# Performance work log

Measured on AMD Instinct MI355X. Metric: run time of the kernel, lower is better.

Reference implementation:

```python
import jax, jax.numpy as jnp
import numpy as np

EPS = 1e-6
D, L, HEADS, FF = 384, 12, 6, 1536


def _ln(x, w, b):
    m = x.mean(-1, keepdims=True)
    v = ((x - m) ** 2).mean(-1, keepdims=True)
    return (x - m) / jnp.sqrt(v + EPS) * w + b


def setup_inputs() -> dict:
    key = jax.random.key(0)
    ks = iter(jax.random.split(key, 16))
    B, Cin, H, W = 16, 7, 192, 640
    N = (H // 16) * (W // 16) + 1  # 481 tokens

    def w(shape, s=0.02):
        return (jax.random.normal(next(ks), shape, jnp.float32) * s)

    return dict(
        input=jax.random.normal(next(ks), (B, Cin, H, W), jnp.float32),
        conv_w=w((D, Cin, 16, 16)),
        conv_b=jnp.zeros((D,), jnp.float32),
        cls_token=w((1, 1, D)),
        pos_embed=w((1, N, D)),
        ln1_w=jnp.ones((L, D), jnp.float32), ln1_b=jnp.zeros((L, D), jnp.float32),
        qkv_w=w((L, 3 * D, D)), qkv_b=jnp.zeros((L, 3 * D), jnp.float32),
        proj_w=w((L, D, D)), proj_b=jnp.zeros((L, D), jnp.float32),
        ln2_w=jnp.ones((L, D), jnp.float32), ln2_b=jnp.zeros((L, D), jnp.float32),
        fc1_w=w((L, FF, D)), fc1_b=jnp.zeros((L, FF), jnp.float32),
        fc2_w=w((L, D, FF)), fc2_b=jnp.zeros((L, D), jnp.float32),
        norm_w=jnp.ones((D,), jnp.float32), norm_b=jnp.zeros((D,), jnp.float32),
        to_qkv_w=w((3 * D, D)),
        pose_w=w((D, D)), pose_b=jnp.zeros((D,), jnp.float32),
    )


def reference(input, conv_w, conv_b, cls_token, pos_embed, ln1_w, ln1_b,
              qkv_w, qkv_b, proj_w, proj_b, ln2_w, ln2_b, fc1_w, fc1_b,
              fc2_w, fc2_b, norm_w, norm_b, to_qkv_w, pose_w, pose_b):
    B = input.shape[0]
    dh = D // HEADS
    # patch embed: conv stride=kernel=16 -> [B,384,12,40] -> [B,480,384]
    x = jax.lax.conv_general_dilated(
        input, conv_w, (16, 16), 'VALID',
        dimension_numbers=('NCHW', 'OIHW', 'NCHW')) + conv_b[None, :, None, None]
    x = x.reshape(B, D, -1).transpose(0, 2, 1)
    x = jnp.concatenate([jnp.broadcast_to(cls_token, (B, 1, D)), x], axis=1) + pos_embed
    # 12 pre-norm ViT blocks (timm vit_small: 6 heads, GELU, eps=1e-6)
    for i in range(L):
        h = _ln(x, ln1_w[i], ln1_b[i])
        qkv = h @ qkv_w[i].T + qkv_b[i]
        q, k, v = jnp.split(qkv, 3, axis=-1)
        hd = lambda t: t.reshape(B, -1, HEADS, dh).transpose(0, 2, 1, 3)
        q, k, v = hd(q) * (dh ** -0.5), hd(k), hd(v)
        a = jax.nn.softmax(jnp.einsum('bhqd,bhkd->bhqk', q, k), axis=-1)
        o = jnp.einsum('bhqk,bhkd->bhqd', a, v).transpose(0, 2, 1, 3).reshape(B, -1, D)
        x = x + o @ proj_w[i].T + proj_b[i]
        h = _ln(x, ln2_w[i], ln2_b[i])
        h = jax.nn.gelu(h @ fc1_w[i].T + fc1_b[i], approximate=False)
        x = x + h @ fc2_w[i].T + fc2_b[i]
    x = _ln(x, norm_w, norm_b)
    # ---- make_pose (training branch: per-column-chunk softmax + median mask) ----
    t = x[:, 1:, :]                      # drop cls -> [B,480,384]
    N = t.shape[1]
    qkv = (t @ to_qkv_w.T).reshape(B, N, 3, D).transpose(2, 0, 1, 3)
    q, k, v = qkv[0] * 0.05103, qkv[1], qkv[2]
    attn = jnp.einsum('bqc,bkc->bqk', q, k) / 100.0
    # col chunk c = columns {c + 40*j : j=0..11}; 40 disjoint chunks of 12
    col_idx = jnp.arange(40)[:, None] + 40 * jnp.arange(12)[None, :]  # [40,12]
    part = jax.nn.softmax(attn[:, :, col_idx], axis=-1)               # [B,N,40,12]
    # torch.median of 12 values = lower median = sorted index (12-1)//2
    med = jnp.sort(part, axis=-1)[..., (12 - 1) // 2][..., None]
    mask = jnp.where(part > med, 0.0, part)
    flat_cols = col_idx.reshape(-1)  # permutation of 0..479
    attn_new = jnp.zeros_like(attn).at[:, :, flat_cols].set(part.reshape(B, N, N))
    masked = jnp.zeros_like(attn).at[:, :, flat_cols].set(mask.reshape(B, N, N))
    masked = masked / ((D // 8) / 2)  # /= num_indices/2 = 24
    # NOTE: einsum 'bal,bnc->bac' shares only 'b': rowsum(attn) outer rowsum(v)
    out = jnp.einsum('bal,bnc->bac', attn_new, v)
    out = out @ pose_w.T + pose_b
    out = _ln(out, norm_w, norm_b)
    attn_map = attn_new.mean(axis=1).reshape(B, 12, 40)
    masked_map = masked.mean(axis=1).reshape(B, 12, 40)
    return out.mean(axis=1), attn_map, masked_map
```

## Files before the change

kernel.cpp:

```cpp
#include <hip/hip_runtime.h>
#include <hip/hip_bf16.h>

#define TD 384
#define NHEAD 6
#define NFF 1536
#define NB 16
#define NTOK 481
#define NROWS (NB*NTOK)

typedef __attribute__((ext_vector_type(8))) __bf16 bf16x8;
typedef __attribute__((ext_vector_type(4))) __bf16 bf16x4;
typedef __attribute__((ext_vector_type(4))) float f32x4;

static __device__ __forceinline__ float gelu_f(float v){
    return 0.5f*v*(1.0f + erff(v*0.70710678118654752f));
}

static __device__ __forceinline__ void gload16(const void* g, void* l){
    __builtin_amdgcn_global_load_lds((const __attribute__((address_space(1))) void*)g,
                                     (__attribute__((address_space(3))) void*)l, 16, 0, 0);
}

template<int ROWS>
static __device__ __forceinline__ void stageT(const __bf16* g, int ldel, __bf16* lds, int w, int lane){
    #pragma unroll
    for (int j = 0; j < ROWS/32; ++j){
        int i = w*(ROWS/32) + j;
        int ol = i*1024 + lane*16;
        int row = ol >> 7, colb = ol & 127;
        int sc = colb ^ ((row & 7) << 4);
        gload16((const char*)g + (long)row*ldel*2 + sc, (char*)lds + i*1024);
    }
}

__global__ __launch_bounds__(256) void mgemm(
    const __bf16* __restrict__ A, int lda, long sA,
    const __bf16* __restrict__ Bm, int ldb, long sB,
    void* __restrict__ Cp, int ldc, long sC,
    const float* __restrict__ bias,
    const float* __restrict__ Rp, long sR,
    int M, int N, int K, float scale, int act, int obf)
{
    __shared__ __align__(16) __bf16 As[2][64*64];
    __shared__ __align__(16) __bf16 Bs[2][64*64];
    const int bz = blockIdx.z;
    A  += (long)bz*sA; Bm += (long)bz*sB;

    const int nwg = gridDim.x*gridDim.y;
    const int id  = blockIdx.y*gridDim.x + blockIdx.x;
    const int q8  = nwg >> 3, r8 = nwg & 7;
    const int xcd = id & 7, sub = id >> 3;
    const int nid = (xcd < r8 ? xcd*(q8+1) : r8*(q8+1) + (xcd-r8)*q8) + sub;
    const int m0 = (nid / gridDim.x) * 64, n0 = (nid % gridDim.x) * 64;

    const int tid = threadIdx.x;
    const int w = tid >> 6, lane = tid & 63;
    const int wr = w >> 1, wc = w & 1;
    const int lr = lane & 15, lg = lane >> 4;

    f32x4 acc[2][2];
    #pragma unroll
    for (int m=0;m<2;++m)
        #pragma unroll
        for (int n=0;n<2;++n)
            acc[m][n] = (f32x4){0.f,0.f,0.f,0.f};

    const __bf16* Ag = A + (long)m0*lda;
    const __bf16* Bg = Bm + (long)n0*ldb;
    const int NT = K >> 6;

    stageT<64>(Ag, lda, As[0], w, lane);
    stageT<64>(Bg, ldb, Bs[0], w, lane);
    int cur = 0;
    for (int t = 0; t < NT; ++t){
        if (t+1 < NT){
            stageT<64>(Ag + (t+1)*64, lda, As[cur^1], w, lane);
            stageT<64>(Bg + (t+1)*64, ldb, Bs[cur^1], w, lane);
            asm volatile("s_waitcnt vmcnt(4)" ::: "memory");
        } else {
            asm volatile("s_waitcnt vmcnt(0)" ::: "memory");
        }
        __builtin_amdgcn_sched_barrier(0);
        __builtin_amdgcn_s_barrier();
        #pragma unroll
        for (int kk=0;kk<2;++kk){
            const int sa = ((kk*64 + lg*16) ^ ((lr&7)<<4));
            bf16x8 af[2], bfr[2];
            #pragma unroll
            for (int m=0;m<2;++m)
                af[m] = *(const bf16x8*)((const char*)&As[cur][0] + (wr*32 + m*16 + lr)*128 + sa);
            #pragma unroll
            for (int n=0;n<2;++n)
                bfr[n] = *(const bf16x8*)((const char*)&Bs[cur][0] + (wc*32 + n*16 + lr)*128 + sa);
            #pragma unroll
            for (int m=0;m<2;++m)
                #pragma unroll
                for (int n=0;n<2;++n)
                    acc[m][n] = __builtin_amdgcn_mfma_f32_16x16x32_bf16(af[m], bfr[n], acc[m][n], 0, 0, 0);
        }
        __builtin_amdgcn_s_barrier();
        cur ^= 1;
    }

    #pragma unroll
    for (int m=0;m<2;++m){
        #pragma unroll
        for (int n=0;n<2;++n){
            int col = n0 + wc*32 + n*16 + lr;
            if (col >= N) continue;
            #pragma unroll
            for (int e=0;e<4;++e){
                int row = m0 + wr*32 + m*16 + lg*4 + e;
                if (row >= M) continue;
                float v = acc[m][n][e]*scale;
                if (bias) v += bias[col];
                if (act) v = gelu_f(v);
                if (Rp) v += Rp[(long)bz*sR + (long)row*ldc + col];
                if (obf) ((__bf16*)Cp)[(long)bz*sC + (long)row*ldc + col] = (__bf16)v;
                else     ((float*)Cp)[(long)bz*sC + (long)row*ldc + col] = v;
            }
        }
    }
}

__global__ __launch_bounds__(256) void attn2(const __bf16* __restrict__ QKV, __bf16* __restrict__ O)
{
    __shared__ __align__(16) __bf16 Ks[64*64];
    __shared__ __align__(16) __bf16 VT[64*72];
    __shared__ __align__(16) __bf16 Ps[64*72];
    const int qt=blockIdx.x, h=blockIdx.y, b=blockIdx.z;
    const int tid=threadIdx.x, w=tid>>6, lane=tid&63;
    const int lr=lane&15, lg=lane>>4;
    const __bf16* base = QKV + (long)b*NTOK*1152;
    const long qrow = qt*64 + w*16 + lr;
    const bf16x8 qa0 = *(const bf16x8*)(base + qrow*1152 + h*64 + lg*8);
    const bf16x8 qa1 = *(const bf16x8*)(base + qrow*1152 + h*64 + 32 + lg*8);

    f32x4 oacc[4];
    float mo[4], lo[4];
    #pragma unroll
    for (int e=0;e<4;++e){ mo[e]=-1e30f; lo[e]=0.f; }
    #pragma unroll
    for (int n=0;n<4;++n) oacc[n]=(f32x4){0.f,0.f,0.f,0.f};

    for (int kt=0; kt<8; ++kt){
        __syncthreads();
        #pragma unroll
        for (int j=0;j<2;++j){
            int i = w*2+j;
            int ol = i*1024 + lane*16;
            int row = ol>>7, colb = ol&127;
            int sc = colb ^ ((row&7)<<4);
            gload16((const char*)base + ((long)(kt*64+row)*1152 + 384 + h*64)*2 + sc,
                    (char*)Ks + i*1024);
        }
        #pragma unroll
        for (int rep=0;rep<2;++rep){
            int c = tid + rep*256;
            int kv = c & 63, d8 = c >> 6;
            bf16x8 vv = *(const bf16x8*)(base + (long)(kt*64+kv)*1152 + 768 + h*64 + d8*8);
            #pragma unroll
            for (int jj=0;jj<8;++jj) VT[(d8*8+jj)*72 + kv] = vv[jj];
        }
        __syncthreads();

        f32x4 s[4];
        #pragma unroll
        for (int n=0;n<4;++n) s[n]=(f32x4){0.f,0.f,0.f,0.f};
        #pragma unroll
        for (int kk=0;kk<2;++kk){
            const int sa = ((kk*64 + lg*16) ^ ((lr&7)<<4));
            #pragma unroll
            for (int n=0;n<4;++n){
                bf16x8 kb = *(const bf16x8*)((const char*)Ks + (n*16+lr)*128 + sa);
                s[n] = __builtin_amdgcn_mfma_f32_16x16x32_bf16(kk? qa1:qa0, kb, s[n], 0,0,0);
            }
        }
        #pragma unroll
        for (int n=0;n<4;++n){
            int col = kt*64 + n*16 + lr;
            bool bad = col >= NTOK;
            #pragma unroll
            for (int e=0;e<4;++e) s[n][e] = bad ? -1e30f : s[n][e]*0.125f;
        }
        #pragma unroll
        for (int e=0;e<4;++e){
            float rm = fmaxf(fmaxf(s[0][e],s[1][e]), fmaxf(s[2][e],s[3][e]));
            rm = fmaxf(rm, __shfl_xor(rm,1));
            rm = fmaxf(rm, __shfl_xor(rm,2));
            rm = fmaxf(rm, __shfl_xor(rm,4));
            rm = fmaxf(rm, __shfl_xor(rm,8));
            float mn = fmaxf(mo[e], rm);
            float al = __expf(mo[e]-mn);
            float rs = 0.f;
            #pragma unroll
            for (int n=0;n<4;++n){ float p=__expf(s[n][e]-mn); s[n][e]=p; rs+=p; }
            rs += __shfl_xor(rs,1); rs += __shfl_xor(rs,2);
            rs += __shfl_xor(rs,4); rs += __shfl_xor(rs,8);
            lo[e] = lo[e]*al + rs; mo[e]=mn;
            #pragma unroll
            for (int n=0;n<4;++n) oacc[n][e] *= al;
        }
        #pragma unroll
        for (int n=0;n<4;++n)
            #pragma unroll
            for (int e=0;e<4;++e)
                Ps[(w*16+lg*4+e)*72 + n*16+lr] = (__bf16)s[n][e];
        #pragma unroll
        for (int kk=0;kk<2;++kk){
            bf16x8 pa = *(const bf16x8*)&Ps[(w*16+lr)*72 + kk*32 + lg*8];
            #pragma unroll
            for (int n=0;n<4;++n){
                bf16x8 vf = *(const bf16x8*)&VT[(n*16+lr)*72 + kk*32 + lg*8];
                oacc[n] = __builtin_amdgcn_mfma_f32_16x16x32_bf16(pa, vf, oacc[n], 0,0,0);
            }
        }
    }
    #pragma unroll
    for (int e=0;e<4;++e){
        int q = qt*64 + w*16 + lg*4 + e;
        if (q < NTOK){
            float inv = 1.f/lo[e];
            __bf16* op = O + ((long)b*NTOK + q)*TD + h*64;
            #pragma unroll
            for (int n=0;n<4;++n)
                op[n*16+lr] = (__bf16)(oacc[n][e]*inv);
        }
    }
}

__global__ __launch_bounds__(128) void ln_kernel(const float* __restrict__ Xp, __bf16* __restrict__ Y,
    const float* __restrict__ W, const float* __restrict__ Bp)
{
    long r = blockIdx.x;
    int t = threadIdx.x;
    const float* x = Xp + r*TD;
    float v0 = x[t], v1 = x[t+128], v2 = x[t+256];
    float s = v0+v1+v2;
    float q = v0*v0+v1*v1+v2*v2;
    #pragma unroll
    for (int w=1; w<64; w<<=1){ s += __shfl_xor(s,w); q += __shfl_xor(q,w); }
    __shared__ float sm[2][2];
    if ((t&63)==0){ sm[t>>6][0]=s; sm[t>>6][1]=q; }
    __syncthreads();
    float S = sm[0][0]+sm[1][0];
    float Q = sm[0][1]+sm[1][1];
    float mean = S*(1.f/384.f);
    float var  = Q*(1.f/384.f) - mean*mean;
    float rstd = rsqrtf(var + 1e-6f);
    __bf16* y = Y + r*TD;
    y[t]     = (__bf16)((v0-mean)*rstd*W[t]     + Bp[t]);
    y[t+128] = (__bf16)((v1-mean)*rstd*W[t+128] + Bp[t+128]);
    y[t+256] = (__bf16)((v2-mean)*rstd*W[t+256] + Bp[t+256]);
}

__global__ void wconv_kernel(const float* __restrict__ s, __bf16* __restrict__ d, int n4){
    int i = blockIdx.x*256 + threadIdx.x;
    if (i < n4){
        float4 v = ((const float4*)s)[i];
        bf16x4 p; p[0]=(__bf16)v.x; p[1]=(__bf16)v.y; p[2]=(__bf16)v.z; p[3]=(__bf16)v.w;
        ((bf16x4*)d)[i] = p;
    }
}

__global__ void im2col_kernel(const float* __restrict__ in, __bf16* __restrict__ outp)
{
    long idx = (long)blockIdx.x*256 + threadIdx.x;
    if (idx >= (long)7680*1792) return;
    int k = (int)(idx % 1792);
    long m = idx / 1792;
    int pw = (int)(m % 40);
    long t2 = m / 40;
    int ph = (int)(t2 % 12);
    int b  = (int)(t2 / 12);
    int kw = k & 15, kh = (k >> 4) & 15, c = k >> 8;
    outp[idx] = (__bf16)in[(((long)(b*7 + c)*192) + ph*16 + kh)*640 + pw*16 + kw];
}

__global__ void assemble_kernel(const float* __restrict__ CO, const float* __restrict__ cls,
    const float* __restrict__ pos, float* __restrict__ X)
{
    long idx = (long)blockIdx.x*256 + threadIdx.x;
    if (idx >= (long)NROWS*TD) return;
    int d = (int)(idx % TD);
    long r = idx / TD;
    int tok = (int)(r % NTOK);
    int b   = (int)(r / NTOK);
    float v = (tok == 0) ? cls[d] : CO[((long)b*480 + tok-1)*TD + d];
    X[idx] = v + pos[tok*TD + d];
}

__global__ __launch_bounds__(256) void pose_maps_kernel(const float* __restrict__ PA,
    float* __restrict__ attn_map, float* __restrict__ masked_map)
{
    int i = blockIdx.x;
    int b = blockIdx.y;
    int t = threadIdx.x;
    float accA[12], accM[12];
    #pragma unroll
    for (int j=0;j<12;++j){ accA[j]=0.f; accM[j]=0.f; }
    for (int a = t; a < 480; a += 256) {
        const float* row = PA + ((long)(b*480 + a))*480 + i;
        float v[12];
        float mx = -1e30f;
        #pragma unroll
        for (int j=0;j<12;++j){ v[j] = row[40*j]; mx = fmaxf(mx, v[j]); }
        float sum = 0.f;
        #pragma unroll
        for (int j=0;j<12;++j){ v[j] = expf(v[j]-mx); sum += v[j]; }
        float invs = 1.f/sum;
        #pragma unroll
        for (int j=0;j<12;++j) v[j] *= invs;
        float srt[12];
        #pragma unroll
        for (int j=0;j<12;++j){
            float x = v[j]; int p = j;
            while (p > 0 && srt[p-1] > x){ srt[p]=srt[p-1]; --p; }
            srt[p]=x;
        }
        float med = srt[5];
        #pragma unroll
        for (int j=0;j<12;++j){
            accA[j] += v[j];
            accM[j] += (v[j] > med) ? 0.f : v[j];
        }
    }
    __shared__ float redA[256*12];
    __shared__ float redM[256*12];
    #pragma unroll
    for (int j=0;j<12;++j){ redA[t*12+j]=accA[j]; redM[t*12+j]=accM[j]; }
    __syncthreads();
    for (int sgap=128; sgap>0; sgap>>=1){
        if (t < sgap){
            #pragma unroll
            for (int j=0;j<12;++j){
                redA[t*12+j] += redA[(t+sgap)*12+j];
                redM[t*12+j] += redM[(t+sgap)*12+j];
            }
        }
        __syncthreads();
    }
    if (t < 12){
        attn_map  [(b*12 + t)*40 + i] = redA[t] * (1.f/480.f);
        masked_map[(b*12 + t)*40 + i] = redM[t] * (1.f/480.f) * (1.f/24.f);
    }
}

__global__ __launch_bounds__(384) void colsum4_kernel(const __bf16* __restrict__ QKV2, float* __restrict__ CS4)
{
    int b = blockIdx.x, j = blockIdx.y, c = threadIdx.x;
    const __bf16* p = QKV2 + (long)b*480*1152 + 768 + c;
    float s = 0.f;
    for (int a = j*120; a < j*120+120; ++a) s += (float)p[(long)a*1152];
    CS4[((long)b*4 + j)*384 + c] = s;
}

__global__ __launch_bounds__(384) void pose_final_kernel(const float* __restrict__ CS4,
    const float* __restrict__ PW, const float* __restrict__ PB,
    const float* __restrict__ NW, const float* __restrict__ NBb, float* __restrict__ out)
{
    int b = blockIdx.x, c = threadIdx.x;
    const float* s0 = CS4 + (long)b*1536;
    __shared__ float sv[384];
    sv[c] = s0[c] + s0[384+c] + s0[768+c] + s0[1152+c];
    __syncthreads();
    const float* wr = PW + (long)c*384;
    float acc = 0.f;
    for (int k = 0; k < 384; ++k) acc += sv[k]*wr[k];
    acc = 40.f*acc + PB[c];
    float s = acc, q = acc*acc;
    #pragma unroll
    for (int w=1; w<64; w<<=1){ s += __shfl_xor(s,w); q += __shfl_xor(q,w); }
    __shared__ float sm[6][2];
    if ((c & 63) == 0){ sm[c>>6][0]=s; sm[c>>6][1]=q; }
    __syncthreads();
    float S=0.f, Q=0.f;
    for (int i=0;i<6;++i){ S+=sm[i][0]; Q+=sm[i][1]; }
    float mean = S*(1.f/384.f);
    float var  = Q*(1.f/384.f) - mean*mean;
    float rstd = rsqrtf(var + 1e-6f);
    out[b*384 + c] = (acc-mean)*rstd*NW[c] + NBb[c];
}

extern "C" void kernel_launch(void* const* d_in, const int* in_sizes, int n_in,
                              void* d_out, int out_size, void* d_ws, size_t ws_size,
                              hipStream_t stream)
{
    const float* input  = (const float*)d_in[0];
    const float* conv_w = (const float*)d_in[1];
    const float* conv_b = (const float*)d_in[2];
    const float* cls    = (const float*)d_in[3];
    const float* pos    = (const float*)d_in[4];
    const float* ln1w   = (const float*)d_in[5];
    const float* ln1b   = (const float*)d_in[6];
    const float* qkvw   = (const float*)d_in[7];
    const float* qkvb   = (const float*)d_in[8];
    const float* projw  = (const float*)d_in[9];
    const float* projb  = (const float*)d_in[10];
    const float* ln2w   = (const float*)d_in[11];
    const float* ln2b   = (const float*)d_in[12];
    const float* fc1w   = (const float*)d_in[13];
    const float* fc1b   = (const float*)d_in[14];
    const float* fc2w   = (const float*)d_in[15];
    const float* fc2b   = (const float*)d_in[16];
    const float* normw  = (const float*)d_in[17];
    const float* normb  = (const float*)d_in[18];
    const float* toqkvw = (const float*)d_in[19];
    const float* posew  = (const float*)d_in[20];
    const float* poseb  = (const float*)d_in[21];
    float* out = (float*)d_out;
    float* ws  = (float*)d_ws;

    __bf16* WB   = (__bf16*)ws;
    float*  X    = ws + 11182080;
    __bf16* Hbf  = (__bf16*)(ws + 14137344);
    __bf16* QKVb = (__bf16*)(ws + 15636480);
    __bf16* Obuf = (__bf16*)(ws + 21633024);
    float*  PAb  = ws + 23132160;
    float*  CS4  = PAb + 3686400;
    __bf16* IM2C = QKVb;

    __bf16* Wconv = WB;
    __bf16* Wqkv  = WB + 688128;
    __bf16* Wproj = WB + 5996544;
    __bf16* Wfc1  = WB + 7766016;
    __bf16* Wfc2  = WB + 14843904;
    __bf16* Wtoq  = WB + 21921792;

    wconv_kernel<<<dim3((172032+255)/256), 256, 0, stream>>>(conv_w, Wconv, 172032);
    wconv_kernel<<<dim3((1327104+255)/256), 256, 0, stream>>>(qkvw,  Wqkv, 1327104);
    wconv_kernel<<<dim3((442368+255)/256), 256, 0, stream>>>(projw, Wproj, 442368);
    wconv_kernel<<<dim3((1769472+255)/256), 256, 0, stream>>>(fc1w,  Wfc1, 1769472);
    wconv_kernel<<<dim3((1769472+255)/256), 256, 0, stream>>>(fc2w,  Wfc2, 1769472);
    wconv_kernel<<<dim3((110592+255)/256), 256, 0, stream>>>(toqkvw, Wtoq, 110592);

    {
        long total = (long)7680*1792;
        im2col_kernel<<<dim3((unsigned)((total+255)/256)), 256, 0, stream>>>(input, IM2C);
    }
    mgemm<<<dim3(6, 120, 1), 256, 0, stream>>>(IM2C, 1792, 0, Wconv, 1792, 0,
        PAb, 384, 0, conv_b, nullptr, 0, 7680, 384, 1792, 1.f, 0, 0);
    assemble_kernel<<<dim3((NROWS*TD+255)/256), 256, 0, stream>>>(PAb, cls, pos, X);

    for (int i = 0; i < 12; ++i) {
        ln_kernel<<<dim3(NROWS), 128, 0, stream>>>(X, Hbf, ln1w + i*384, ln1b + i*384);
        mgemm<<<dim3(18, 121, 1), 256, 0, stream>>>(Hbf, 384, 0, Wqkv + (long)i*1152*384, 384, 0,
            QKVb, 1152, 0, qkvb + i*1152, nullptr, 0, NROWS, 1152, 384, 1.f, 0, 1);
        attn2<<<dim3(8, NHEAD, NB), 256, 0, stream>>>(QKVb, Obuf);
        mgemm<<<dim3(6, 121, 1), 256, 0, stream>>>(Obuf, 384, 0, Wproj + (long)i*384*384, 384, 0,
            X, 384, 0, projb + i*384, X, 0, NROWS, 384, 384, 1.f, 0, 0);
        ln_kernel<<<dim3(NROWS), 128, 0, stream>>>(X, Hbf, ln2w + i*384, ln2b + i*384);
        mgemm<<<dim3(24, 121, 1), 256, 0, stream>>>(Hbf, 384, 0, Wfc1 + (long)i*1536*384, 384, 0,
            QKVb, 1536, 0, fc1b + i*1536, nullptr, 0, NROWS, 1536, 384, 1.f, 1, 1);
        mgemm<<<dim3(6, 121, 1), 256, 0, stream>>>(QKVb, 1536, 0, Wfc2 + (long)i*384*1536, 1536, 0,
            X, 384, 0, fc2b + i*384, X, 0, NROWS, 384, 1536, 1.f, 0, 0);
    }
    ln_kernel<<<dim3(NROWS), 128, 0, stream>>>(X, Hbf, normw, normb);

    mgemm<<<dim3(18, 8, 16), 256, 0, stream>>>(Hbf + 384, 384, (long)481*384,
        Wtoq, 384, 0, QKVb, 1152, (long)480*1152, nullptr, nullptr, 0, 480, 1152, 384, 1.f, 0, 1);
    mgemm<<<dim3(8, 8, 16), 256, 0, stream>>>(QKVb, 1152, (long)480*1152,
        QKVb + 384, 1152, (long)480*1152, PAb, 480, (long)480*480, nullptr, nullptr, 0,
        480, 480, 384, 0.05103f*0.01f, 0, 0);
    pose_maps_kernel<<<dim3(40, 16), 256, 0, stream>>>(PAb, out + 6144, out + 13824);
    colsum4_kernel<<<dim3(16, 4), 384, 0, stream>>>(QKVb, CS4);
    pose_final_kernel<<<dim3(16), 384, 0, stream>>>(CS4, posew, poseb, normw, normb, out);
}
```

Before: 1.805 ms.

## Fold LayerNorm into GEMM epilogues and double-buffer K/V loads in attention

LayerNorm weights are folded into the QKV, FC1 and to_qkv weight matrices. The mean and rstd correction is applied in the GEMM epilogue from per-row stats computed by a light stats kernel over a bf16 copy of the residual stream, which the residual GEMMs now also write. This drops the separate normalized-activation write and read each layer. The attention kernel also double-buffers K tiles and prefetches V into registers to overlap loads with MFMA compute. The risk is precision: the GEMM now consumes unnormalized bf16 activations, and the mean subtraction happens after accumulation, so cancellation can occur.

```diff
diff --git a/kernel.cpp b/kernel.cpp
--- a/kernel.cpp
+++ b/kernel.cpp
@@ -39,6 +39,8 @@
     void* __restrict__ Cp, int ldc, long sC,
     const float* __restrict__ bias,
     const float* __restrict__ Rp, long sR,
+    const float2* __restrict__ MR, long sMR, const float2* __restrict__ SB2,
+    __bf16* __restrict__ Xbp,
     int M, int N, int K, float scale, int act, int obf)
 {
     __shared__ __align__(16) __bf16 As[2][64*64];
@@ -105,19 +107,27 @@
     #pragma unroll
     for (int m=0;m<2;++m){
         #pragma unroll
-        for (int n=0;n<2;++n){
-            int col = n0 + wc*32 + n*16 + lr;
-            if (col >= N) continue;
-            #pragma unroll
-            for (int e=0;e<4;++e){
-                int row = m0 + wr*32 + m*16 + lg*4 + e;
-                if (row >= M) continue;
-                float v = acc[m][n][e]*scale;
-                if (bias) v += bias[col];
+        for (int e=0;e<4;++e){
+            int row = m0 + wr*32 + m*16 + lg*4 + e;
+            if (row >= M) continue;
+            float2 mr = MR ? MR[(long)bz*sMR + row] : make_float2(0.f,0.f);
+            #pragma unroll
+            for (int n=0;n<2;++n){
+                int col = n0 + wc*32 + n*16 + lr;
+                if (col >= N) continue;
+                float v = acc[m][n][e];
+                if (MR){
+                    float2 sb = SB2[col];
+                    v = mr.y*(v - mr.x*sb.x) + sb.y;
+                } else {
+                    v = v*scale;
+                    if (bias) v += bias[col];
+                }
                 if (act) v = gelu_f(v);
                 if (Rp) v += Rp[(long)bz*sR + (long)row*ldc + col];
                 if (obf) ((__bf16*)Cp)[(long)bz*sC + (long)row*ldc + col] = (__bf16)v;
                 else     ((float*)Cp)[(long)bz*sC + (long)row*ldc + col] = v;
+                if (Xbp) Xbp[(long)row*ldc + col] = (__bf16)v;
             }
         }
     }
@@ -125,17 +135,29 @@
 
 __global__ __launch_bounds__(256) void attn2(const __bf16* __restrict__ QKV, __bf16* __restrict__ O)
 {
-    __shared__ __align__(16) __bf16 Ks[64*64];
+    __shared__ __align__(16) __bf16 Ks[2][64*64];
     __shared__ __align__(16) __bf16 VT[64*72];
     __shared__ __align__(16) __bf16 Ps[64*72];
     const int qt=blockIdx.x, h=blockIdx.y, b=blockIdx.z;
     const int tid=threadIdx.x, w=tid>>6, lane=tid&63;
     const int lr=lane&15, lg=lane>>4;
+    const int kv0 = tid & 63, d80 = tid >> 6;
     const __bf16* base = QKV + (long)b*NTOK*1152;
     const long qrow = qt*64 + w*16 + lr;
     const bf16x8 qa0 = *(const bf16x8*)(base + qrow*1152 + h*64 + lg*8);
     const bf16x8 qa1 = *(const bf16x8*)(base + qrow*1152 + h*64 + 32 + lg*8);
 
+    #pragma unroll
+    for (int j=0;j<2;++j){
+        int i = w*2+j;
+        int ol = i*1024 + lane*16;
+        int row = ol>>7, colb = ol&127;
+        int sc = colb ^ ((row&7)<<4);
+        gload16((const char*)base + ((long)row*1152 + 384 + h*64)*2 + sc, (char*)Ks[0] + i*1024);
+    }
+    bf16x8 vv0 = *(const bf16x8*)(base + (long)kv0*1152 + 768 + h*64 + d80*8);
+    bf16x8 vv1 = *(const bf16x8*)(base + (long)kv0*1152 + 768 + h*64 + (d80+4)*8);
+
     f32x4 oacc[4];
     float mo[4], lo[4];
     #pragma unroll
@@ -143,26 +165,30 @@
     #pragma unroll
     for (int n=0;n<4;++n) oacc[n]=(f32x4){0.f,0.f,0.f,0.f};
 
+    int cur = 0;
     for (int kt=0; kt<8; ++kt){
-        __syncthreads();
-        #pragma unroll
-        for (int j=0;j<2;++j){
-            int i = w*2+j;
-            int ol = i*1024 + lane*16;
-            int row = ol>>7, colb = ol&127;
-            int sc = colb ^ ((row&7)<<4);
-            gload16((const char*)base + ((long)(kt*64+row)*1152 + 384 + h*64)*2 + sc,
-                    (char*)Ks + i*1024);
-        }
-        #pragma unroll
-        for (int rep=0;rep<2;++rep){
-            int c = tid + rep*256;
-            int kv = c & 63, d8 = c >> 6;
-            bf16x8 vv = *(const bf16x8*)(base + (long)(kt*64+kv)*1152 + 768 + h*64 + d8*8);
-            #pragma unroll
-            for (int jj=0;jj<8;++jj) VT[(d8*8+jj)*72 + kv] = vv[jj];
-        }
-        __syncthreads();
+        asm volatile("s_waitcnt vmcnt(0)" ::: "memory");
+        __builtin_amdgcn_sched_barrier(0);
+        #pragma unroll
+        for (int jj=0;jj<8;++jj) VT[(d80*8+jj)*72 + kv0] = vv0[jj];
+        #pragma unroll
+        for (int jj=0;jj<8;++jj) VT[((d80+4)*8+jj)*72 + kv0] = vv1[jj];
+        if (kt+1 < 8){
+            #pragma unroll
+            for (int j=0;j<2;++j){
+                int i = w*2+j;
+                int ol = i*1024 + lane*16;
+                int row = ol>>7, colb = ol&127;
+                int sc = colb ^ ((row&7)<<4);
+                gload16((const char*)base + ((long)((kt+1)*64+row)*1152 + 384 + h*64)*2 + sc,
+                        (char*)Ks[cur^1] + i*1024);
+            }
+            vv0 = *(const bf16x8*)(base + (long)((kt+1)*64+kv0)*1152 + 768 + h*64 + d80*8);
+            vv1 = *(const bf16x8*)(base + (long)((kt+1)*64+kv0)*1152 + 768 + h*64 + (d80+4)*8);
+        }
+        asm volatile("s_waitcnt lgkmcnt(0)" ::: "memory");
+        __builtin_amdgcn_sched_barrier(0);
+        __builtin_amdgcn_s_barrier();
 
         f32x4 s[4];
         #pragma unroll
@@ -172,7 +198,7 @@
             const int sa = ((kk*64 + lg*16) ^ ((lr&7)<<4));
             #pragma unroll
             for (int n=0;n<4;++n){
-                bf16x8 kb = *(const bf16x8*)((const char*)Ks + (n*16+lr)*128 + sa);
+                bf16x8 kb = *(const bf16x8*)((const char*)&Ks[cur][0] + (n*16+lr)*128 + sa);
                 s[n] = __builtin_amdgcn_mfma_f32_16x16x32_bf16(kk? qa1:qa0, kb, s[n], 0,0,0);
             }
         }
@@ -215,6 +241,8 @@
                 oacc[n] = __builtin_amdgcn_mfma_f32_16x16x32_bf16(pa, vf, oacc[n], 0,0,0);
             }
         }
+        __builtin_amdgcn_s_barrier();
+        cur ^= 1;
     }
     #pragma unroll
     for (int e=0;e<4;++e){
@@ -229,29 +257,63 @@
     }
 }
 
-__global__ __launch_bounds__(128) void ln_kernel(const float* __restrict__ Xp, __bf16* __restrict__ Y,
-    const float* __restrict__ W, const float* __restrict__ Bp)
-{
-    long r = blockIdx.x;
-    int t = threadIdx.x;
-    const float* x = Xp + r*TD;
-    float v0 = x[t], v1 = x[t+128], v2 = x[t+256];
-    float s = v0+v1+v2;
-    float q = v0*v0+v1*v1+v2*v2;
-    #pragma unroll
-    for (int w=1; w<64; w<<=1){ s += __shfl_xor(s,w); q += __shfl_xor(q,w); }
-    __shared__ float sm[2][2];
-    if ((t&63)==0){ sm[t>>6][0]=s; sm[t>>6][1]=q; }
-    __syncthreads();
-    float S = sm[0][0]+sm[1][0];
-    float Q = sm[0][1]+sm[1][1];
-    float mean = S*(1.f/384.f);
-    float var  = Q*(1.f/384.f) - mean*mean;
-    float rstd = rsqrtf(var + 1e-6f);
-    __bf16* y = Y + r*TD;
-    y[t]     = (__bf16)((v0-mean)*rstd*W[t]     + Bp[t]);
-    y[t+128] = (__bf16)((v1-mean)*rstd*W[t+128] + Bp[t+128]);
-    y[t+256] = (__bf16)((v2-mean)*rstd*W[t+256] + Bp[t+256]);
+__global__ __launch_bounds__(256) void stats_kernel(const __bf16* __restrict__ Xb, float2* __restrict__ MR, int nrows)
+{
+    int row = blockIdx.x*4 + (threadIdx.x>>6);
+    if (row >= nrows) return;
+    int lane = threadIdx.x & 63;
+    const uint* p = (const uint*)(Xb + (long)row*384) + lane*3;
+    float s=0.f, q=0.f;
+    #pragma unroll
+    for (int i=0;i<3;++i){
+        uint u = p[i];
+        float a = __uint_as_float(u<<16);
+        float b = __uint_as_float(u & 0xFFFF0000u);
+        s += a+b; q += a*a + b*b;
+    }
+    #pragma unroll
+    for (int d=1; d<64; d<<=1){ s += __shfl_xor(s,d); q += __shfl_xor(q,d); }
+    if (lane==0){
+        float mu = s*(1.f/384.f);
+        float var = q*(1.f/384.f) - mu*mu;
+        MR[row] = make_float2(mu, rsqrtf(var + 1e-6f));
+    }
+}
+
+__global__ void wfold_kernel(const float* __restrict__ s, const float* __restrict__ lnw,
+                             __bf16* __restrict__ d, int n4, int per_layer4)
+{
+    int i = blockIdx.x*256 + threadIdx.x;
+    if (i >= n4) return;
+    int layer = i / per_layer4;
+    int k = (i*4) % 384;
+    float4 v = ((const float4*)s)[i];
+    const float4 lw = *(const float4*)(lnw + layer*384 + k);
+    bf16x4 p; p[0]=(__bf16)(v.x*lw.x); p[1]=(__bf16)(v.y*lw.y); p[2]=(__bf16)(v.z*lw.z); p[3]=(__bf16)(v.w*lw.w);
+    ((bf16x4*)d)[i] = p;
+}
+
+__global__ __launch_bounds__(256) void rowsum_kernel(const float* __restrict__ W,
+    const float* __restrict__ lnw, const float* __restrict__ lnb, const float* __restrict__ bias,
+    float2* __restrict__ SB2, int nrows, int rows_per_layer)
+{
+    int row = blockIdx.x*4 + (threadIdx.x>>6);
+    if (row >= nrows) return;
+    int lane = threadIdx.x & 63;
+    int layer = row / rows_per_layer;
+    const float* wr = W + (long)row*384;
+    const float* lw = lnw + layer*384;
+    const float* lb = lnb + layer*384;
+    float s=0.f, t=0.f;
+    #pragma unroll
+    for (int i=0;i<6;++i){
+        int k = lane + i*64;
+        float wv = wr[k];
+        s += lw[k]*wv; t += lb[k]*wv;
+    }
+    #pragma unroll
+    for (int d=1; d<64; d<<=1){ s += __shfl_xor(s,d); t += __shfl_xor(t,d); }
+    if (lane==0) SB2[row] = make_float2(s, bias ? t + bias[row] : t);
 }
 
 __global__ void wconv_kernel(const float* __restrict__ s, __bf16* __restrict__ d, int n4){
@@ -278,7 +340,7 @@
 }
 
 __global__ void assemble_kernel(const float* __restrict__ CO, const float* __restrict__ cls,
-    const float* __restrict__ pos, float* __restrict__ X)
+    const float* __restrict__ pos, float* __restrict__ X, __bf16* __restrict__ Xb)
 {
     long idx = (long)blockIdx.x*256 + threadIdx.x;
     if (idx >= (long)NROWS*TD) return;
@@ -287,7 +349,9 @@
     int tok = (int)(r % NTOK);
     int b   = (int)(r / NTOK);
     float v = (tok == 0) ? cls[d] : CO[((long)b*480 + tok-1)*TD + d];
-    X[idx] = v + pos[tok*TD + d];
+    v += pos[tok*TD + d];
+    X[idx] = v;
+    Xb[idx] = (__bf16)v;
 }
 
 __global__ __launch_bounds__(256) void pose_maps_kernel(const float* __restrict__ PA,
@@ -411,14 +475,18 @@
     float* out = (float*)d_out;
     float* ws  = (float*)d_ws;
 
-    __bf16* WB   = (__bf16*)ws;
-    float*  X    = ws + 11182080;
-    __bf16* Hbf  = (__bf16*)(ws + 14137344);
-    __bf16* QKVb = (__bf16*)(ws + 15636480);
-    __bf16* Obuf = (__bf16*)(ws + 21633024);
-    float*  PAb  = ws + 23132160;
-    float*  CS4  = PAb + 3686400;
-    __bf16* IM2C = QKVb;
+    __bf16* WB    = (__bf16*)ws;
+    float*  X     = ws + 11182080;
+    __bf16* Xb    = (__bf16*)(ws + 14137344);
+    __bf16* QKVb  = (__bf16*)(ws + 15636480);
+    __bf16* Obuf  = (__bf16*)(ws + 21633024);
+    float*  PAb   = ws + 23132160;
+    float*  CS4   = PAb + 3686400;
+    float2* MR    = (float2*)(ws + 26843136);
+    float2* SB2q  = (float2*)(ws + 26858752);
+    float2* SB2f  = (float2*)(ws + 26886400);
+    float2* SB2t  = (float2*)(ws + 26923264);
+    __bf16* IM2C  = QKVb;
 
     __bf16* Wconv = WB;
     __bf16* Wqkv  = WB + 688128;
@@ -428,40 +496,48 @@
     __bf16* Wtoq  = WB + 21921792;
 
     wconv_kernel<<<dim3((172032+255)/256), 256, 0, stream>>>(conv_w, Wconv, 172032);
-    wconv_kernel<<<dim3((1327104+255)/256), 256, 0, stream>>>(qkvw,  Wqkv, 1327104);
     wconv_kernel<<<dim3((442368+255)/256), 256, 0, stream>>>(projw, Wproj, 442368);
-    wconv_kernel<<<dim3((1769472+255)/256), 256, 0, stream>>>(fc1w,  Wfc1, 1769472);
     wconv_kernel<<<dim3((1769472+255)/256), 256, 0, stream>>>(fc2w,  Wfc2, 1769472);
-    wconv_kernel<<<dim3((110592+255)/256), 256, 0, stream>>>(toqkvw, Wtoq, 110592);
+    wfold_kernel<<<dim3((1327104+255)/256), 256, 0, stream>>>(qkvw, ln1w, Wqkv, 1327104, 110592);
+    wfold_kernel<<<dim3((1769472+255)/256), 256, 0, stream>>>(fc1w, ln2w, Wfc1, 1769472, 147456);
+    wfold_kernel<<<dim3((110592+255)/256), 256, 0, stream>>>(toqkvw, normw, Wtoq, 110592, 110592);
+    rowsum_kernel<<<dim3(13824/4), 256, 0, stream>>>(qkvw, ln1w, ln1b, qkvb, SB2q, 13824, 1152);
+    rowsum_kernel<<<dim3(18432/4), 256, 0, stream>>>(fc1w, ln2w, ln2b, fc1b, SB2f, 18432, 1536);
+    rowsum_kernel<<<dim3(1152/4), 256, 0, stream>>>(toqkvw, normw, normb, nullptr, SB2t, 1152, 1152);
 
     {
         long total = (long)7680*1792;
         im2col_kernel<<<dim3((unsigned)((total+255)/256)), 256, 0, stream>>>(input, IM2C);
     }
     mgemm<<<dim3(6, 120, 1), 256, 0, stream>>>(IM2C, 1792, 0, Wconv, 1792, 0,
-        PAb, 384, 0, conv_b, nullptr, 0, 7680, 384, 1792, 1.f, 0, 0);
-    assemble_kernel<<<dim3((NROWS*TD+255)/256), 256, 0, stream>>>(PAb, cls, pos, X);
+        PAb, 384, 0, conv_b, nullptr, 0, nullptr, 0, nullptr, nullptr, 7680, 384, 1792, 1.f, 0, 0);
+    assemble_kernel<<<dim3((NROWS*TD+255)/256), 256, 0, stream>>>(PAb, cls, pos, X, Xb);
 
     for (int i = 0; i < 12; ++i) {
-        ln_kernel<<<dim3(NROWS), 128, 0, stream>>>(X, Hbf, ln1w + i*384, ln1b + i*384);
-        mgemm<<<dim3(18, 121, 1), 256, 0, stream>>>(Hbf, 384, 0, Wqkv + (long)i*1152*384, 384, 0,
-            QKVb, 1152, 0, qkvb + i*1152, nullptr, 0, NROWS, 1152, 384, 1.f, 0, 1);
+        stats_kernel<<<dim3((NROWS+3)/4), 256, 0, stream>>>(Xb, MR, NROWS);
+        mgemm<<<dim3(18, 121, 1), 256, 0, stream>>>(Xb, 384, 0, Wqkv + (long)i*1152*384, 384, 0,
+            QKVb, 1152, 0, nullptr, nullptr, 0, MR, 0, SB2q + (long)i*1152, nullptr,
+            NROWS, 1152, 384, 1.f, 0, 1);
         attn2<<<dim3(8, NHEAD, NB), 256, 0, stream>>>(QKVb, Obuf);
         mgemm<<<dim3(6, 121, 1), 256, 0, stream>>>(Obuf, 384, 0, Wproj + (long)i*384*384, 384, 0,
-            X, 384, 0, projb + i*384, X, 0, NROWS, 384, 384, 1.f, 0, 0);
-        ln_kernel<<<dim3(NROWS), 128, 0, stream>>>(X, Hbf, ln2w + i*384, ln2b + i*384);
-        mgemm<<<dim3(24, 121, 1), 256, 0, stream>>>(Hbf, 384, 0, Wfc1 + (long)i*1536*384, 384, 0,
-            QKVb, 1536, 0, fc1b + i*1536, nullptr, 0, NROWS, 1536, 384, 1.f, 1, 1);
+            X, 384, 0, projb + i*384, X, 0, nullptr, 0, nullptr, Xb,
+            NROWS, 384, 384, 1.f, 0, 0);
+        stats_kernel<<<dim3((NROWS+3)/4), 256, 0, stream>>>(Xb, MR, NROWS);
+        mgemm<<<dim3(24, 121, 1), 256, 0, stream>>>(Xb, 384, 0, Wfc1 + (long)i*1536*384, 384, 0,
+            QKVb, 1536, 0, nullptr, nullptr, 0, MR, 0, SB2f + (long)i*1536, nullptr,
+            NROWS, 1536, 384, 1.f, 1, 1);
         mgemm<<<dim3(6, 121, 1), 256, 0, stream>>>(QKVb, 1536, 0, Wfc2 + (long)i*384*1536, 1536, 0,
-            X, 384, 0, fc2b + i*384, X, 0, NROWS, 384, 1536, 1.f, 0, 0);
-    }
-    ln_kernel<<<dim3(NROWS), 128, 0, stream>>>(X, Hbf, normw, normb);
-
-    mgemm<<<dim3(18, 8, 16), 256, 0, stream>>>(Hbf + 384, 384, (long)481*384,
-        Wtoq, 384, 0, QKVb, 1152, (long)480*1152, nullptr, nullptr, 0, 480, 1152, 384, 1.f, 0, 1);
+            X, 384, 0, fc2b + i*384, X, 0, nullptr, 0, nullptr, Xb,
+            NROWS, 384, 1536, 1.f, 0, 0);
+    }
+
+    stats_kernel<<<dim3((NROWS+3)/4), 256, 0, stream>>>(Xb, MR, NROWS);
+    mgemm<<<dim3(18, 8, 16), 256, 0, stream>>>(Xb + 384, 384, (long)481*384,
+        Wtoq, 384, 0, QKVb, 1152, (long)480*1152, nullptr, nullptr, 0,
+        MR + 1, 481, SB2t, nullptr, 480, 1152, 384, 1.f, 0, 1);
     mgemm<<<dim3(8, 8, 16), 256, 0, stream>>>(QKVb, 1152, (long)480*1152,
         QKVb + 384, 1152, (long)480*1152, PAb, 480, (long)480*480, nullptr, nullptr, 0,
-        480, 480, 384, 0.05103f*0.01f, 0, 0);
+        nullptr, 0, nullptr, nullptr, 480, 480, 384, 0.05103f*0.01f, 0, 0);
     pose_maps_kernel<<<dim3(40, 16), 256, 0, stream>>>(PAb, out + 6144, out + 13824);
     colsum4_kernel<<<dim3(16, 4), 384, 0, stream>>>(QKVb, CS4);
     pose_final_kernel<<<dim3(16), 384, 0, stream>>>(CS4, posew, poseb, normw, normb, out);
```

Measured after the change: 2.003 ms. +11.0%, slower.

## Add weight-stationary persistent GEMM for K=384 projections with double-buffered A tiles

Applied to the files above, without the earlier changes.

Adds a wgemm kernel in which each block keeps its 128-column slice of the weight matrix (the full K=384) in registers. The block then loops persistently over 32-row A tiles, using async global-to-LDS loads into a double-buffered, XOR-swizzled shared buffer, with an XCD-aware remap of block ids. It replaces mgemm for the QKV, proj, fc1, to_qkv and attention-score GEMMs, aiming to avoid reloading weights for every output tile and to overlap A loads with MFMA work. The cost is high register use for the resident weights (launch bounds of 3 blocks per CU). It also hardcodes K=384, and when N is not a multiple of 128 it reads weight rows past N.

```diff
diff --git a/kernel.cpp b/kernel.cpp
--- a/kernel.cpp
+++ b/kernel.cpp
@@ -118,6 +118,121 @@
                 if (Rp) v += Rp[(long)bz*sR + (long)row*ldc + col];
                 if (obf) ((__bf16*)Cp)[(long)bz*sC + (long)row*ldc + col] = (__bf16)v;
                 else     ((float*)Cp)[(long)bz*sC + (long)row*ldc + col] = v;
+            }
+        }
+    }
+}
+
+__global__ __launch_bounds__(256, 3) void wgemm(
+    const __bf16* __restrict__ A, int lda, long sA,
+    const __bf16* __restrict__ Bm, int ldb, long sB,
+    void* __restrict__ Cp, int ldc, long sC,
+    const float* __restrict__ bias,
+    const float* __restrict__ Rp, long sR,
+    int M, int N, float scale, int act, int obf)
+{
+    __shared__ __align__(16) __bf16 As[2][32*384];
+    const int bz = blockIdx.z;
+    A  += (long)bz*sA; Bm += (long)bz*sB;
+
+    const int nwg = gridDim.x*gridDim.y;
+    const int id  = blockIdx.y*gridDim.x + blockIdx.x;
+    const int q8  = nwg >> 3, r8 = nwg & 7;
+    const int xcd = id & 7, sub = id >> 3;
+    const int nid = (xcd < r8 ? xcd*(q8+1) : r8*(q8+1) + (xcd-r8)*q8) + sub;
+    const int gx = nid % gridDim.x, gy = nid / gridDim.x;
+    const int n0 = gx*128;
+
+    const int tid = threadIdx.x;
+    const int w = tid >> 6, lane = tid & 63;
+    const int lr = lane & 15, lg = lane >> 4;
+
+    const int MT = (M + 31) >> 5;
+    if (gy >= MT) return;
+
+    bf16x8 breg[2][12];
+    {
+        const __bf16* B0 = Bm + (long)(n0 + w*32 + lr)*ldb + lg*8;
+        #pragma unroll
+        for (int kk=0; kk<12; ++kk){
+            breg[0][kk] = *(const bf16x8*)(B0 + kk*32);
+            breg[1][kk] = *(const bf16x8*)(B0 + 16*ldb + kk*32);
+        }
+    }
+
+    const int gdy = gridDim.y;
+    int t = 0;
+    {
+        const char* g0 = (const char*)(A + (long)gy*32*lda);
+        #pragma unroll
+        for (int j=0;j<6;++j){
+            int i = w*6 + j;
+            int s = i >> 2, qq = i & 3;
+            int ol = qq*1024 + lane*16;
+            int row = ol >> 7, colb = ol & 127;
+            int sc = colb ^ ((row & 7) << 4);
+            gload16(g0 + (long)row*lda*2 + s*128 + sc, (char*)As[0] + i*1024);
+        }
+    }
+
+    for (int mt = gy; mt < MT; mt += gdy, ++t){
+        int nmt = mt + gdy;
+        if (nmt < MT){
+            const char* g1 = (const char*)(A + (long)nmt*32*lda);
+            #pragma unroll
+            for (int j=0;j<6;++j){
+                int i = w*6 + j;
+                int s = i >> 2, qq = i & 3;
+                int ol = qq*1024 + lane*16;
+                int row = ol >> 7, colb = ol & 127;
+                int sc = colb ^ ((row & 7) << 4);
+                gload16(g1 + (long)row*lda*2 + s*128 + sc, (char*)As[(t+1)&1] + i*1024);
+            }
+            asm volatile("s_waitcnt vmcnt(6)" ::: "memory");
+        } else {
+            asm volatile("s_waitcnt vmcnt(0)" ::: "memory");
+        }
+        __builtin_amdgcn_sched_barrier(0);
+        __builtin_amdgcn_s_barrier();
+
+        const char* Ab = (const char*)As[t&1];
+        f32x4 acc[2][2];
+        #pragma unroll
+        for (int m=0;m<2;++m)
+            #pragma unroll
+            for (int n=0;n<2;++n)
+                acc[m][n] = (f32x4){0.f,0.f,0.f,0.f};
+
+        #pragma unroll
+        for (int kk=0; kk<12; ++kk){
+            const int s = kk >> 1;
+            const int sa = (((kk&1)*64 + lg*16) ^ ((lr&7)<<4));
+            bf16x8 a0 = *(const bf16x8*)(Ab + s*4096 + (lr)*128 + sa);
+            bf16x8 a1 = *(const bf16x8*)(Ab + s*4096 + (16+lr)*128 + sa);
+            acc[0][0] = __builtin_amdgcn_mfma_f32_16x16x32_bf16(a0, breg[0][kk], acc[0][0], 0,0,0);
+            acc[0][1] = __builtin_amdgcn_mfma_f32_16x16x32_bf16(a0, breg[1][kk], acc[0][1], 0,0,0);
+            acc[1][0] = __builtin_amdgcn_mfma_f32_16x16x32_bf16(a1, breg[0][kk], acc[1][0], 0,0,0);
+            acc[1][1] = __builtin_amdgcn_mfma_f32_16x16x32_bf16(a1, breg[1][kk], acc[1][1], 0,0,0);
+        }
+        __builtin_amdgcn_s_barrier();
+
+        #pragma unroll
+        for (int m=0;m<2;++m){
+            #pragma unroll
+            for (int n=0;n<2;++n){
+                int col = n0 + w*32 + n*16 + lr;
+                if (col >= N) continue;
+                #pragma unroll
+                for (int e=0;e<4;++e){
+                    int row = mt*32 + m*16 + lg*4 + e;
+                    if (row >= M) continue;
+                    float v = acc[m][n][e]*scale;
+                    if (bias) v += bias[col];
+                    if (act) v = gelu_f(v);
+                    if (Rp) v += Rp[(long)bz*sR + (long)row*ldc + col];
+                    if (obf) ((__bf16*)Cp)[(long)bz*sC + (long)row*ldc + col] = (__bf16)v;
+                    else     ((float*)Cp)[(long)bz*sC + (long)row*ldc + col] = v;
+                }
             }
         }
     }
@@ -444,24 +559,24 @@
 
     for (int i = 0; i < 12; ++i) {
         ln_kernel<<<dim3(NROWS), 128, 0, stream>>>(X, Hbf, ln1w + i*384, ln1b + i*384);
-        mgemm<<<dim3(18, 121, 1), 256, 0, stream>>>(Hbf, 384, 0, Wqkv + (long)i*1152*384, 384, 0,
-            QKVb, 1152, 0, qkvb + i*1152, nullptr, 0, NROWS, 1152, 384, 1.f, 0, 1);
+        wgemm<<<dim3(9, 86, 1), 256, 0, stream>>>(Hbf, 384, 0, Wqkv + (long)i*1152*384, 384, 0,
+            QKVb, 1152, 0, qkvb + i*1152, nullptr, 0, NROWS, 1152, 1.f, 0, 1);
         attn2<<<dim3(8, NHEAD, NB), 256, 0, stream>>>(QKVb, Obuf);
-        mgemm<<<dim3(6, 121, 1), 256, 0, stream>>>(Obuf, 384, 0, Wproj + (long)i*384*384, 384, 0,
-            X, 384, 0, projb + i*384, X, 0, NROWS, 384, 384, 1.f, 0, 0);
+        wgemm<<<dim3(3, 241, 1), 256, 0, stream>>>(Obuf, 384, 0, Wproj + (long)i*384*384, 384, 0,
+            X, 384, 0, projb + i*384, X, 0, NROWS, 384, 1.f, 0, 0);
         ln_kernel<<<dim3(NROWS), 128, 0, stream>>>(X, Hbf, ln2w + i*384, ln2b + i*384);
-        mgemm<<<dim3(24, 121, 1), 256, 0, stream>>>(Hbf, 384, 0, Wfc1 + (long)i*1536*384, 384, 0,
-            QKVb, 1536, 0, fc1b + i*1536, nullptr, 0, NROWS, 1536, 384, 1.f, 1, 1);
+        wgemm<<<dim3(12, 64, 1), 256, 0, stream>>>(Hbf, 384, 0, Wfc1 + (long)i*1536*384, 384, 0,
+            QKVb, 1536, 0, fc1b + i*1536, nullptr, 0, NROWS, 1536, 1.f, 1, 1);
         mgemm<<<dim3(6, 121, 1), 256, 0, stream>>>(QKVb, 1536, 0, Wfc2 + (long)i*384*1536, 1536, 0,
             X, 384, 0, fc2b + i*384, X, 0, NROWS, 384, 1536, 1.f, 0, 0);
     }
     ln_kernel<<<dim3(NROWS), 128, 0, stream>>>(X, Hbf, normw, normb);
 
-    mgemm<<<dim3(18, 8, 16), 256, 0, stream>>>(Hbf + 384, 384, (long)481*384,
-        Wtoq, 384, 0, QKVb, 1152, (long)480*1152, nullptr, nullptr, 0, 480, 1152, 384, 1.f, 0, 1);
-    mgemm<<<dim3(8, 8, 16), 256, 0, stream>>>(QKVb, 1152, (long)480*1152,
+    wgemm<<<dim3(9, 5, 16), 256, 0, stream>>>(Hbf + 384, 384, (long)481*384,
+        Wtoq, 384, 0, QKVb, 1152, (long)480*1152, nullptr, nullptr, 0, 480, 1152, 1.f, 0, 1);
+    wgemm<<<dim3(4, 8, 16), 256, 0, stream>>>(QKVb, 1152, (long)480*1152,
         QKVb + 384, 1152, (long)480*1152, PAb, 480, (long)480*480, nullptr, nullptr, 0,
-        480, 480, 384, 0.05103f*0.01f, 0, 0);
+        480, 480, 0.05103f*0.01f, 0, 0);
     pose_maps_kernel<<<dim3(40, 16), 256, 0, stream>>>(PAb, out + 6144, out + 13824);
     colsum4_kernel<<<dim3(16, 4), 384, 0, stream>>>(QKVb, CS4);
     pose_final_kernel<<<dim3(16), 384, 0, stream>>>(CS4, posew, poseb, normw, normb, out);
```

New measurement: 2.069 ms. 14.6% more time.

## Replace LDS-staged GEMM with direct register-loaded MFMA GEMM

Applied to the files above, without the earlier changes.

Drops the shared-memory double-buffered staging in the GEMM kernel. Each lane now loads its MFMA A/B fragments straight from global memory into registers, 128 K at a time. This removes LDS traffic and workgroup barriers. The cost is that the four waves no longer share tiles, so each wave reads its own data from global memory and leans on L1/L2 for reuse, with less latency hiding than explicit prefetching. Rows past M in the last tile block are also read without bounds checks.

```diff
diff --git a/kernel.cpp b/kernel.cpp
--- a/kernel.cpp
+++ b/kernel.cpp
@@ -21,19 +21,7 @@
                                      (__attribute__((address_space(3))) void*)l, 16, 0, 0);
 }
 
-template<int ROWS>
-static __device__ __forceinline__ void stageT(const __bf16* g, int ldel, __bf16* lds, int w, int lane){
-    #pragma unroll
-    for (int j = 0; j < ROWS/32; ++j){
-        int i = w*(ROWS/32) + j;
-        int ol = i*1024 + lane*16;
-        int row = ol >> 7, colb = ol & 127;
-        int sc = colb ^ ((row & 7) << 4);
-        gload16((const char*)g + (long)row*ldel*2 + sc, (char*)lds + i*1024);
-    }
-}
-
-__global__ __launch_bounds__(256) void mgemm(
+__global__ __launch_bounds__(256) void rgemm(
     const __bf16* __restrict__ A, int lda, long sA,
     const __bf16* __restrict__ Bm, int ldb, long sB,
     void* __restrict__ Cp, int ldc, long sC,
@@ -41,8 +29,6 @@
     const float* __restrict__ Rp, long sR,
     int M, int N, int K, float scale, int act, int obf)
 {
-    __shared__ __align__(16) __bf16 As[2][64*64];
-    __shared__ __align__(16) __bf16 Bs[2][64*64];
     const int bz = blockIdx.z;
     A  += (long)bz*sA; Bm += (long)bz*sB;
 
@@ -58,6 +44,11 @@
     const int wr = w >> 1, wc = w & 1;
     const int lr = lane & 15, lg = lane >> 4;
 
+    const __bf16* Ap0 = A  + (long)(m0 + wr*32 + lr)*lda + lg*8;
+    const __bf16* Ap1 = Ap0 + (long)16*lda;
+    const __bf16* Bp0 = Bm + (long)(n0 + wc*32 + lr)*ldb + lg*8;
+    const __bf16* Bp1 = Bp0 + (long)16*ldb;
+
     f32x4 acc[2][2];
     #pragma unroll
     for (int m=0;m<2;++m)
@@ -65,41 +56,23 @@
         for (int n=0;n<2;++n)
             acc[m][n] = (f32x4){0.f,0.f,0.f,0.f};
 
-    const __bf16* Ag = A + (long)m0*lda;
-    const __bf16* Bg = Bm + (long)n0*ldb;
-    const int NT = K >> 6;
-
-    stageT<64>(Ag, lda, As[0], w, lane);
-    stageT<64>(Bg, ldb, Bs[0], w, lane);
-    int cur = 0;
-    for (int t = 0; t < NT; ++t){
-        if (t+1 < NT){
-            stageT<64>(Ag + (t+1)*64, lda, As[cur^1], w, lane);
-            stageT<64>(Bg + (t+1)*64, ldb, Bs[cur^1], w, lane);
-            asm volatile("s_waitcnt vmcnt(4)" ::: "memory");
-        } else {
-            asm volatile("s_waitcnt vmcnt(0)" ::: "memory");
-        }
-        __builtin_amdgcn_sched_barrier(0);
-        __builtin_amdgcn_s_barrier();
-        #pragma unroll
-        for (int kk=0;kk<2;++kk){
-            const int sa = ((kk*64 + lg*16) ^ ((lr&7)<<4));
-            bf16x8 af[2], bfr[2];
-            #pragma unroll
-            for (int m=0;m<2;++m)
-                af[m] = *(const bf16x8*)((const char*)&As[cur][0] + (wr*32 + m*16 + lr)*128 + sa);
-            #pragma unroll
-            for (int n=0;n<2;++n)
-                bfr[n] = *(const bf16x8*)((const char*)&Bs[cur][0] + (wc*32 + n*16 + lr)*128 + sa);
-            #pragma unroll
-            for (int m=0;m<2;++m)
-                #pragma unroll
-                for (int n=0;n<2;++n)
-                    acc[m][n] = __builtin_amdgcn_mfma_f32_16x16x32_bf16(af[m], bfr[n], acc[m][n], 0, 0, 0);
-        }
-        __builtin_amdgcn_s_barrier();
-        cur ^= 1;
+    #pragma unroll 2
+    for (int k0 = 0; k0 < K; k0 += 128){
+        bf16x8 a0[4], a1[4], b0[4], b1[4];
+        #pragma unroll
+        for (int kk=0;kk<4;++kk){
+            a0[kk] = *(const bf16x8*)(Ap0 + k0 + kk*32);
+            a1[kk] = *(const bf16x8*)(Ap1 + k0 + kk*32);
+            b0[kk] = *(const bf16x8*)(Bp0 + k0 + kk*32);
+            b1[kk] = *(const bf16x8*)(Bp1 + k0 + kk*32);
+        }
+        #pragma unroll
+        for (int kk=0;kk<4;++kk){
+            acc[0][0] = __builtin_amdgcn_mfma_f32_16x16x32_bf16(a0[kk], b0[kk], acc[0][0], 0,0,0);
+            acc[0][1] = __builtin_amdgcn_mfma_f32_16x16x32_bf16(a0[kk], b1[kk], acc[0][1], 0,0,0);
+            acc[1][0] = __builtin_amdgcn_mfma_f32_16x16x32_bf16(a1[kk], b0[kk], acc[1][0], 0,0,0);
+            acc[1][1] = __builtin_amdgcn_mfma_f32_16x16x32_bf16(a1[kk], b1[kk], acc[1][1], 0,0,0);
+        }
     }
 
     #pragma unroll
@@ -438,28 +411,28 @@
         long total = (long)7680*1792;
         im2col_kernel<<<dim3((unsigned)((total+255)/256)), 256, 0, stream>>>(input, IM2C);
     }
-    mgemm<<<dim3(6, 120, 1), 256, 0, stream>>>(IM2C, 1792, 0, Wconv, 1792, 0,
+    rgemm<<<dim3(6, 120, 1), 256, 0, stream>>>(IM2C, 1792, 0, Wconv, 1792, 0,
         PAb, 384, 0, conv_b, nullptr, 0, 7680, 384, 1792, 1.f, 0, 0);
     assemble_kernel<<<dim3((NROWS*TD+255)/256), 256, 0, stream>>>(PAb, cls, pos, X);
 
     for (int i = 0; i < 12; ++i) {
         ln_kernel<<<dim3(NROWS), 128, 0, stream>>>(X, Hbf, ln1w + i*384, ln1b + i*384);
-        mgemm<<<dim3(18, 121, 1), 256, 0, stream>>>(Hbf, 384, 0, Wqkv + (long)i*1152*384, 384, 0,
+        rgemm<<<dim3(18, 121, 1), 256, 0, stream>>>(Hbf, 384, 0, Wqkv + (long)i*1152*384, 384, 0,
             QKVb, 1152, 0, qkvb + i*1152, nullptr, 0, NROWS, 1152, 384, 1.f, 0, 1);
         attn2<<<dim3(8, NHEAD, NB), 256, 0, stream>>>(QKVb, Obuf);
-        mgemm<<<dim3(6, 121, 1), 256, 0, stream>>>(Obuf, 384, 0, Wproj + (long)i*384*384, 384, 0,
+        rgemm<<<dim3(6, 121, 1), 256, 0, stream>>>(Obuf, 384, 0, Wproj + (long)i*384*384, 384, 0,
             X, 384, 0, projb + i*384, X, 0, NROWS, 384, 384, 1.f, 0, 0);
         ln_kernel<<<dim3(NROWS), 128, 0, stream>>>(X, Hbf, ln2w + i*384, ln2b + i*384);
-        mgemm<<<dim3(24, 121, 1), 256, 0, stream>>>(Hbf, 384, 0, Wfc1 + (long)i*1536*384, 384, 0,
+        rgemm<<<dim3(24, 121, 1), 256, 0, stream>>>(Hbf, 384, 0, Wfc1 + (long)i*1536*384, 384, 0,
             QKVb, 1536, 0, fc1b + i*1536, nullptr, 0, NROWS, 1536, 384, 1.f, 1, 1);
-        mgemm<<<dim3(6, 121, 1), 256, 0, stream>>>(QKVb, 1536, 0, Wfc2 + (long)i*384*1536, 1536, 0,
+        rgemm<<<dim3(6, 121, 1), 256, 0, stream>>>(QKVb, 1536, 0, Wfc2 + (long)i*384*1536, 1536, 0,
             X, 384, 0, fc2b + i*384, X, 0, NROWS, 384, 1536, 1.f, 0, 0);
     }
     ln_kernel<<<dim3(NROWS), 128, 0, stream>>>(X, Hbf, normw, normb);
 
-    mgemm<<<dim3(18, 8, 16), 256, 0, stream>>>(Hbf + 384, 384, (long)481*384,
+    rgemm<<<dim3(18, 8, 16), 256, 0, stream>>>(Hbf + 384, 384, (long)481*384,
         Wtoq, 384, 0, QKVb, 1152, (long)480*1152, nullptr, nullptr, 0, 480, 1152, 384, 1.f, 0, 1);
-    mgemm<<<dim3(8, 8, 16), 256, 0, stream>>>(QKVb, 1152, (long)480*1152,
+    rgemm<<<dim3(8, 8, 16), 256, 0, stream>>>(QKVb, 1152, (long)480*1152,
         QKVb + 384, 1152, (long)480*1152, PAb, 480, (long)480*480, nullptr, nullptr, 0,
         480, 480, 384, 0.05103f*0.01f, 0, 0);
     pose_maps_kernel<<<dim3(40, 16), 256, 0, stream>>>(PAb, out + 6144, out + 13824);
```

Result: slower. 3.518 ms (+95.0%).
